# Kernel optimization log

Hardware: AMD Instinct MI355X
Metric: run time of the kernel (lower is better)

## Reference

```python
import jax, jax.numpy as jnp
import numpy as np
import math

B, S, H = 2, 2048, 2048
NH, HD = 32, 64
BASE, SCALE = 10000.0, 2.0
MAX_POS, ORIG_MAX_POS = 8192, 8192
BETA_FAST, BETA_SLOW = 32, 1
EPS = 1e-6


def _yarn_cos_sin():
    # revised_yarn: scale inv_freq by 1/((1-mask)*scale + mask)
    inv_freq = 1.0 / BASE ** (np.arange(0, HD, 2, dtype=np.float64) / HD)
    def corr(nr):
        return HD * math.log(ORIG_MAX_POS / (nr * 2 * math.pi)) / (2 * math.log(BASE))
    low = max(math.floor(corr(BETA_FAST)), 0)
    high = min(math.ceil(corr(BETA_SLOW)), HD - 1)
    hi = high + 0.001 if low == high else high
    ramp = np.clip((np.arange(HD // 2, dtype=np.float64) - low) / (hi - low), 0.0, 1.0)
    mask = 1.0 - ramp  # extrapolation_factor = 1
    inv_freq = inv_freq / ((1.0 - mask) * SCALE + mask)
    mscale = (0.1 * math.log(SCALE) + 1.0) if SCALE > 1 else 1.0
    t = np.arange(MAX_POS, dtype=np.float64)
    freqs = np.outer(t, inv_freq)
    emb = np.concatenate([freqs, freqs], axis=-1)
    return np.cos(emb) * mscale, np.sin(emb) * mscale

_COS_NP, _SIN_NP = _yarn_cos_sin()


def rotate_half(x):
    x1, x2 = jnp.split(x, 2, axis=-1)
    return jnp.concatenate([-x2, x1], axis=-1)


def rms_norm(x, w):
    v = jnp.mean(jnp.square(x.astype(jnp.float32)), axis=-1, keepdims=True)
    return (x.astype(jnp.float32) * jax.lax.rsqrt(v + EPS)).astype(x.dtype) * w


def localized_filtering(x, lf1, lf2, w1, b1, w2, b2, ln_w):
    # x: (B,S,H); torch works in (B,H,S,1) with kernel-(2,1) convs over seq
    residual = x
    xi = jnp.transpose(x, (0, 2, 1))[:, :, :, None]  # (B,H,S,1)
    xi = jnp.concatenate([lf1, xi], axis=2)          # (B,H,S+1,1)
    dn = ('NCHW', 'OIHW', 'NCHW')
    o1 = jax.lax.conv_general_dilated(xi, w1, (1, 1), 'VALID', dimension_numbers=dn)
    o1 = o1 + b1[None, :, None, None]                # (B,H/2,S,1)
    o1c = jnp.concatenate([lf2, o1], axis=2)         # (B,H/2,S+1,1)
    o2 = jax.lax.conv_general_dilated(o1c, w2, (1, 1), 'VALID', dimension_numbers=dn)
    o2 = o2 + b2[None, :, None, None]                # (B,H,S,1)
    o2 = jnp.transpose(o2[:, :, :, 0], (0, 2, 1))    # (B,S,H)
    return rms_norm(o2 + residual, ln_w)


def setup_inputs():
    key = jax.random.key(0)
    ks = jax.random.split(key, 8)
    f = lambda k, shp: jax.random.normal(k, shp, dtype=jnp.float32) * 0.02
    return {
        'hidden_states': jax.random.normal(ks[0], (B, S, H), dtype=jnp.float32),
        'position_ids': jnp.broadcast_to(jnp.arange(S, dtype=jnp.int32)[None, :], (B, S)),
        'lf1_cache': jnp.zeros((B, H, 1, 1), jnp.float32),
        'lf2_cache': jnp.zeros((B, H // 2, 1, 1), jnp.float32),
        'Wqk': f(ks[1], (2 * H, H)),
        'Wv': f(ks[2], (H, H)),
        'Wo': f(ks[3], (H, H)),
        'conv1_w': f(ks[4], (H // 2, H, 2, 1)),
        'conv1_b': jnp.zeros((H // 2,), jnp.float32),
        'conv2_w': f(ks[5], (H, H // 2, 2, 1)),
        'conv2_b': jnp.zeros((H,), jnp.float32),
        'ln_w': jnp.ones((H,), jnp.float32),
    }


def reference(hidden_states, position_ids, lf1_cache, lf2_cache, Wqk, Wv, Wo,
              conv1_w, conv1_b, conv2_w, conv2_b, ln_w):
    cos = jnp.asarray(_COS_NP, jnp.float32)
    sin = jnp.asarray(_SIN_NP, jnp.float32)
    # v from raw hidden states
    v = (hidden_states @ Wv.T).reshape(B, S, NH, HD).transpose(0, 2, 1, 3)  # (B,NH,S,HD)
    # localized filtering gate feeds q/k projection
    lf = localized_filtering(hidden_states, lf1_cache, lf2_cache,
                             conv1_w, conv1_b, conv2_w, conv2_b, ln_w)
    qk = (lf @ Wqk.T).reshape(B, S, NH, 2 * HD)  # per-head [q|k] split
    q = qk[..., :HD].transpose(0, 2, 1, 3)       # (B,NH,S,HD)
    k = qk[..., HD:].transpose(0, 2, 1, 3)
    cos_p = cos[position_ids][:, None, :, :]     # (B,1,S,HD)
    sin_p = sin[position_ids][:, None, :, :]
    q = q * cos_p + rotate_half(q) * sin_p
    k = k * cos_p + rotate_half(k) * sin_p
    scores = jnp.einsum('bhqd,bhkd->bhqk', q, k) / math.sqrt(HD)
    causal = jnp.tril(jnp.ones((S, S), dtype=bool))
    scores = jnp.where(causal[None, None], scores, jnp.finfo(scores.dtype).min)
    attn = jax.nn.softmax(scores, axis=-1)
    ctx = jnp.einsum('bhqk,bhkd->bhqd', attn, v)
    out = ctx.transpose(0, 2, 1, 3).reshape(B, S, H) @ Wo.T
    return out
```

## Files before the change

### kernel.cpp

```cpp
#include <hip/hip_runtime.h>
#include <hip/hip_bf16.h>
#include <math.h>
#include <stdint.h>

typedef __hip_bfloat16 bf16;
using f32x4 = __attribute__((ext_vector_type(4))) float;
using s16x8 = __attribute__((ext_vector_type(8))) short;

constexpr int Bc = 2, Sc = 2048, Hc = 2048, NHc = 32, HDc = 64;
constexpr int Mc = Bc * Sc;
constexpr int MAXPOS = 8192;

constexpr size_t OFF_WV  = 0;
constexpr size_t OFF_WQK = OFF_WV  + (size_t)Hc * Hc * 2;
constexpr size_t OFF_WO  = OFF_WQK + (size_t)2 * Hc * Hc * 2;
constexpr size_t OFF_W1  = OFF_WO  + (size_t)Hc * Hc * 2;
constexpr size_t OFF_W2  = OFF_W1  + (size_t)(Hc/2) * (2*Hc) * 2;
constexpr size_t OFF_HS  = OFF_W2  + (size_t)Hc * Hc * 2;
constexpr size_t OFF_XPR = OFF_HS  + (size_t)Mc * Hc * 2;
constexpr size_t OFF_O1  = OFF_XPR + (size_t)Mc * Hc * 2;
constexpr size_t OFF_O1P = OFF_O1  + (size_t)Mc * (Hc/2) * 2;
constexpr size_t OFF_O2  = OFF_O1P + (size_t)Mc * (Hc/2) * 2;
constexpr size_t OFF_LF  = OFF_O2  + (size_t)Mc * Hc * 4;
constexpr size_t OFF_VT  = OFF_LF  + (size_t)Mc * Hc * 2;
constexpr size_t OFF_COS = OFF_VT  + (size_t)Mc * Hc * 2;
constexpr size_t OFF_SIN = OFF_COS + (size_t)MAXPOS * HDc * 4;
constexpr size_t OFF_Q   = OFF_XPR;
constexpr size_t OFF_K   = OFF_HS;
constexpr size_t OFF_CTX = OFF_O1;

__device__ __forceinline__ f32x4 mfma16(s16x8 a, s16x8 b, f32x4 c) {
  return __builtin_amdgcn_mfma_f32_16x16x32_bf16(a, b, c, 0, 0, 0);
}
__device__ __forceinline__ void gload16(const bf16* g, bf16* l) {
  __builtin_amdgcn_global_load_lds(
      (__attribute__((address_space(1))) void*)g,
      (__attribute__((address_space(3))) void*)l, 16, 0, 0);
}
__device__ __forceinline__ uint16_t bfbits(float x) {
  union { bf16 h; uint16_t u; } v; v.h = __float2bfloat16(x); return v.u;
}
__device__ __forceinline__ uint32_t pkbf(float a, float b) {
  return (uint32_t)bfbits(a) | ((uint32_t)bfbits(b) << 16);
}
__device__ __forceinline__ void block_bar() {
  asm volatile("" ::: "memory");
  __builtin_amdgcn_s_barrier();
  asm volatile("" ::: "memory");
}
template <int N> __device__ __forceinline__ void vm_wait() {
  if constexpr (N == 0)      asm volatile("s_waitcnt vmcnt(0)" ::: "memory");
  else if constexpr (N == 2) asm volatile("s_waitcnt vmcnt(2)" ::: "memory");
  else if constexpr (N == 3) asm volatile("s_waitcnt vmcnt(3)" ::: "memory");
  else if constexpr (N == 4) asm volatile("s_waitcnt vmcnt(4)" ::: "memory");
  else if constexpr (N == 6) asm volatile("s_waitcnt vmcnt(6)" ::: "memory");
  else if constexpr (N == 8) asm volatile("s_waitcnt vmcnt(8)" ::: "memory");
}

__global__ void k_cvt(const float* __restrict__ in, bf16* __restrict__ out, int n) {
  int i = blockIdx.x * 256 + threadIdx.x;
  if (i < n) out[i] = __float2bfloat16(in[i]);
}

__global__ void k_cvt_hs(const float* __restrict__ hs, const float* __restrict__ lf1,
                         bf16* __restrict__ hsb, bf16* __restrict__ xprev) {
  int i = blockIdx.x * 256 + threadIdx.x;
  if (i >= Mc * Hc) return;
  float v = hs[i];
  bf16 b = __float2bfloat16(v);
  hsb[i] = b;
  int row = i >> 11, col = i & (Hc - 1);
  int s = row & (Sc - 1), bb = row >> 11;
  if (s + 1 < Sc) xprev[i + Hc] = b;
  if (s == 0)     xprev[i] = __float2bfloat16(lf1[bb * Hc + col]);
}

__global__ void k_repack1(const float* __restrict__ w, bf16* __restrict__ out) {
  int i = blockIdx.x * 256 + threadIdx.x;
  if (i >= (Hc/2) * 2 * Hc) return;
  int oc = i >> 12, k = i & 4095;
  int ic = k & (Hc - 1), t = k >> 11;
  out[i] = __float2bfloat16(w[((size_t)oc * Hc + ic) * 2 + t]);
}
__global__ void k_repack2(const float* __restrict__ w, bf16* __restrict__ out) {
  int i = blockIdx.x * 256 + threadIdx.x;
  if (i >= Hc * Hc) return;
  int c = i >> 11, k = i & (Hc - 1);
  int oc = k & (Hc/2 - 1), t = k >> 10;
  out[i] = __float2bfloat16(w[((size_t)c * (Hc/2) + oc) * 2 + t]);
}

__global__ void k_prefill_o1p(const float* __restrict__ lf2, bf16* __restrict__ o1p) {
  int i = blockIdx.x * 256 + threadIdx.x;
  if (i >= Bc * (Hc/2)) return;
  int b = i >> 10, n = i & (Hc/2 - 1);
  o1p[(size_t)b * Sc * (Hc/2) + n] = __float2bfloat16(lf2[i]);
}

struct InvF { double v[32]; double mscale; };

__global__ void k_costab(InvF f, float* __restrict__ ct, float* __restrict__ st) {
  int i = blockIdx.x * 256 + threadIdx.x;
  if (i >= MAXPOS * HDc) return;
  int p = i >> 6, d = i & 63;
  double ang = (double)p * f.v[d & 31];
  ct[i] = (float)(cos(ang) * f.mscale);
  st[i] = (float)(sin(ang) * f.mscale);
}

__global__ __launch_bounds__(256) void k_rmsnorm(const float* __restrict__ x,
                                                 const float* __restrict__ w,
                                                 bf16* __restrict__ out) {
  __shared__ float red[4];
  int row = blockIdx.x;
  const float* xr = x + (size_t)row * Hc;
  float ss = 0.f;
  for (int c = threadIdx.x; c < Hc; c += 256) { float v = xr[c]; ss += v * v; }
  for (int off = 32; off; off >>= 1) ss += __shfl_down(ss, off, 64);
  if ((threadIdx.x & 63) == 0) red[threadIdx.x >> 6] = ss;
  __syncthreads();
  float sc = rsqrtf((red[0] + red[1] + red[2] + red[3]) / Hc + 1e-6f);
  for (int c = threadIdx.x; c < Hc; c += 256)
    out[(size_t)row * Hc + c] = __float2bfloat16(xr[c] * sc * w[c]);
}

template <int EPI, int BM, int BN>
__global__ __launch_bounds__(512, 2) void gemm8(
    const bf16* __restrict__ A0, const bf16* __restrict__ A1, int Ksplit,
    const bf16* __restrict__ Bw, int K, int N, void* __restrict__ Cout,
    const float* __restrict__ bias, const float* __restrict__ resid,
    const int* __restrict__ pos, const float* __restrict__ ct,
    const float* __restrict__ st, bf16* __restrict__ out2) {
  constexpr int L = (BM + BN) / 128;
  constexpr int TILE = (BM + BN) * 32;
  constexpr int MF = (BM == 256) ? ((BN == 256) ? 8 : 4) : 4;
  constexpr int NF = (BN == 256) ? 4 : ((BM == 256) ? 4 : 2);
  __shared__ __align__(16) bf16 lds[3][TILE];
  const int tid = threadIdx.x;
  const int w = tid >> 6, l = tid & 63;
  const int lrow = l & 15, lg = l >> 4;
  const int wm = (BM == 256) ? ((BN == 256) ? (w >> 2) * 128 : (w & 3) * 64)
                             : (w >> 2) * 64;
  const int wn = (BM == 256) ? ((BN == 256) ? (w & 3) * 64 : (w >> 2) * 64)
                             : (w & 3) * 32;
  const int gx = gridDim.x;
  const int lin = blockIdx.y * gx + blockIdx.x;
  const int cx = gx >> 2, cy = gridDim.y >> 1;
  const int c = lin & 7, idx = lin >> 3;
  const int bn = (c & 3) * cx + idx % cx;
  const int bm = (c >> 2) * cy + idx / cx;

  auto ld1 = [&](const bf16* srcbase, size_t stride, bf16* ldst, int ci) {
    const int pr = ci >> 3, rem = ci & 7;
    const int r = pr * 2 + (rem >> 2), g = (rem & 3) ^ (pr & 3);
    gload16(srcbase + (size_t)r * stride + g * 8, ldst + ci * 8);
  };
  auto stage = [&](int kt, int slot) {
    const int kcol = kt * 32;
    const bf16* Au; int kc;
    if (kcol < Ksplit) { Au = A0; kc = kcol; } else { Au = A1; kc = kcol - Ksplit; }
    const bf16* As_ = Au + (size_t)bm * BM * Ksplit + kc;
    bf16* ldsA = lds[slot];
    ld1(As_, Ksplit, ldsA, tid);
    if constexpr (BM == 256) ld1(As_, Ksplit, ldsA, tid + 512);
    const bf16* Bs_ = Bw + (size_t)bn * BN * K + kcol;
    bf16* ldsB = lds[slot] + BM * 32;
    ld1(Bs_, K, ldsB, tid);
    if constexpr (BN == 256) ld1(Bs_, K, ldsB, tid + 512);
  };
  auto frag = [&](const bf16* base, int r) -> s16x8 {
    const int s = ((r >> 1) << 3) + ((r & 1) << 2) + (lg ^ ((r >> 1) & 3));
    return *(const s16x8*)(base + s * 8);
  };

  f32x4 acc[MF][NF] = {};
  const int nkt = K / 32;
  stage(0, 0);
  stage(1, 1);
  for (int t = 0; t < nkt; ++t) {
    if (t + 2 < nkt) { stage(t + 2, (t + 2) % 3); vm_wait<2 * L>(); }
    else if (t + 1 < nkt) { vm_wait<L>(); }
    else { vm_wait<0>(); }
    block_bar();
    const bf16* Asl = lds[t % 3];
    const bf16* Bsl = Asl + BM * 32;
    s16x8 af[MF], bfr[NF];
#pragma unroll
    for (int m = 0; m < MF; ++m) af[m] = frag(Asl, wm + m * 16 + lrow);
#pragma unroll
    for (int n = 0; n < NF; ++n) bfr[n] = frag(Bsl, wn + n * 16 + lrow);
    __builtin_amdgcn_s_setprio(1);
#pragma unroll
    for (int m = 0; m < MF; ++m)
#pragma unroll
      for (int n = 0; n < NF; ++n)
        acc[m][n] = mfma16(af[m], bfr[n], acc[m][n]);
    __builtin_amdgcn_s_setprio(0);
    block_bar();
  }
  if constexpr (EPI == 6) {
    const int gcol0 = bn * BN + wn;
    const int h = gcol0 >> 7, half = (gcol0 >> 6) & 1;
    bf16* outp = half ? out2 : (bf16*)Cout;
    const float qsc = half ? 1.0f : 0.125f * 1.44269504088896f;
#pragma unroll
    for (int m = 0; m < MF; ++m)
#pragma unroll
      for (int r = 0; r < 4; ++r) {
        const int grow = bm * BM + wm + m * 16 + lg * 4 + r;
        const int p = pos[grow];
        const int bb = grow >> 11, s = grow & (Sc - 1);
        bf16* rowp = outp + ((size_t)(bb * NHc + h) * Sc + s) * 64;
#pragma unroll
        for (int n = 0; n < 2; ++n) {
          const int dd = n * 16 + lrow;
          const float c0 = ct[p * 64 + dd],      s0 = st[p * 64 + dd];
          const float c1 = ct[p * 64 + 32 + dd], s1 = st[p * 64 + 32 + dd];
          const float v0 = acc[m][n][r], v1 = acc[m][n + 2][r];
          rowp[dd]      = __float2bfloat16((v0 * c0 - v1 * s0) * qsc);
          rowp[dd + 32] = __float2bfloat16((v1 * c1 + v0 * s1) * qsc);
        }
      }
  } else {
#pragma unroll
    for (int m = 0; m < MF; ++m)
#pragma unroll
      for (int n = 0; n < NF; ++n)
#pragma unroll
        for (int r = 0; r < 4; ++r) {
          const int grow = bm * BM + wm + m * 16 + lg * 4 + r;
          const int gcol = bn * BN + wn + n * 16 + lrow;
          float v = acc[m][n][r];
          if constexpr (EPI == 1) {
            v += bias[gcol];
            bf16 bv = __float2bfloat16(v);
            ((bf16*)Cout)[(size_t)grow * N + gcol] = bv;
            if ((grow & (Sc - 1)) != Sc - 1) out2[(size_t)(grow + 1) * N + gcol] = bv;
          } else if constexpr (EPI == 2) {
            v += bias[gcol] + resid[(size_t)grow * N + gcol];
            ((float*)Cout)[(size_t)grow * N + gcol] = v;
          } else if constexpr (EPI == 5) {
            const int b = gcol >> 11, s = gcol & (Sc - 1);
            ((bf16*)Cout)[((size_t)(b * Hc + grow)) * Sc + s] = __float2bfloat16(v);
          } else {
            ((float*)Cout)[(size_t)grow * N + gcol] = v;
          }
        }
  }
}

__global__ __launch_bounds__(256) void k_attn(const bf16* __restrict__ Q,
                                              const bf16* __restrict__ Kg,
                                              const bf16* __restrict__ Vt,
                                              bf16* __restrict__ ctx) {
  __shared__ __align__(16) bf16 Ks[2][64 * 64];
  __shared__ __align__(16) bf16 Vs[2][64 * 64];
  __shared__ __align__(16) uint32_t Pl[4][2][2][16][20];
  const int tid = threadIdx.x;
  const int w = tid >> 6, l = tid & 63;
  const int lrow = l & 15, lg = l >> 4, lk = lg * 8;
  const int bh = blockIdx.x;
  const int tile = blockIdx.y;
  const bf16* Qp = Q  + (size_t)bh * Sc * HDc;
  const bf16* Kp = Kg + (size_t)bh * Sc * HDc;
  const bf16* Vp = Vt + (size_t)bh * HDc * Sc;
  const int b = bh >> 5, h = bh & 31;
  const s16x8 ones8 = {16256, 16256, 16256, 16256, 16256, 16256, 16256, 16256};

  const int srow0 = tid >> 3, schunk = tid & 7;

  for (int pass = 0; pass < 2; ++pass) {
    const int base = (pass == 0) ? tile * 128 : (Sc - 128 - tile * 128);
    const int q0 = base + w * 32;
    const int NT = base / 64 + 2;

    s16x8 qa[2][2];
#pragma unroll
    for (int m = 0; m < 2; ++m)
#pragma unroll
      for (int hf = 0; hf < 2; ++hf)
        qa[m][hf] = *(const s16x8*)&Qp[(size_t)(q0 + m * 16 + lrow) * 64 + hf * 32 + lk];

    f32x4 o[2][4] = {};
    f32x4 lsf[2] = {};
    float mx[2] = {-1e30f, -1e30f};

    {
      gload16(Kp + (size_t)srow0 * 64 + ((schunk ^ (srow0 & 7)) << 3), &Ks[0][tid * 8]);
      gload16(Kp + (size_t)(32 + srow0) * 64 + ((schunk ^ ((32 + srow0) & 7)) << 3),
              &Ks[0][2048 + tid * 8]);
      gload16(Vp + (size_t)srow0 * Sc + ((schunk ^ (srow0 & 7)) << 3), &Vs[0][tid * 8]);
      gload16(Vp + (size_t)(32 + srow0) * Sc + ((schunk ^ ((32 + srow0) & 7)) << 3),
              &Vs[0][2048 + tid * 8]);
    }
    __syncthreads();

    for (int t = 0; t < NT; ++t) {
      const int cur = t & 1;
      const int kv0 = t * 64;
      if (t + 1 < NT) {
        const int nkv = kv0 + 64;
        const int nb = cur ^ 1;
        gload16(Kp + (size_t)(nkv + srow0) * 64 + ((schunk ^ (srow0 & 7)) << 3),
                &Ks[nb][tid * 8]);
        gload16(Kp + (size_t)(nkv + 32 + srow0) * 64 + ((schunk ^ ((32 + srow0) & 7)) << 3),
                &Ks[nb][2048 + tid * 8]);
        gload16(Vp + (size_t)srow0 * Sc + nkv + ((schunk ^ (srow0 & 7)) << 3),
                &Vs[nb][tid * 8]);
        gload16(Vp + (size_t)(32 + srow0) * Sc + nkv + ((schunk ^ ((32 + srow0) & 7)) << 3),
                &Vs[nb][2048 + tid * 8]);
      }
      if (kv0 <= q0) {
        s16x8 kc[8], vc[4][2];
#pragma unroll
        for (int c = 0; c < 4; ++c)
#pragma unroll
          for (int hf = 0; hf < 2; ++hf) {
            const int row = c * 16 + lrow;
            kc[c * 2 + hf] =
                *(const s16x8*)&Ks[cur][row * 64 + (((hf << 2) + lg) ^ (row & 7)) * 8];
          }
#pragma unroll
        for (int db = 0; db < 4; ++db)
#pragma unroll
          for (int kh = 0; kh < 2; ++kh) {
            const int row = db * 16 + lrow;
            vc[db][kh] =
                *(const s16x8*)&Vs[cur][row * 64 + (((kh << 2) + lg) ^ (row & 7)) * 8];
          }
        const bool lastit = (kv0 + 64 > q0);

#pragma unroll
        for (int m = 0; m < 2; ++m) {
          f32x4 s[4];
          __builtin_amdgcn_s_setprio(1);
#pragma unroll
          for (int c = 0; c < 4; ++c) {
            f32x4 z = {};
            z = mfma16(kc[c * 2], qa[m][0], z);
            z = mfma16(kc[c * 2 + 1], qa[m][1], z);
            s[c] = z;
          }
          __builtin_amdgcn_s_setprio(0);

          if (lastit) {
            const int qq = q0 + m * 16 + lrow;
#pragma unroll
            for (int c = 0; c < 4; ++c)
#pragma unroll
              for (int r = 0; r < 4; ++r)
                if (kv0 + c * 16 + lg * 4 + r > qq) s[c][r] = -1e30f;
          }
          float t16 = fmaxf(
              fmaxf(fmaxf(fmaxf(s[0][0], s[0][1]), fmaxf(s[0][2], s[0][3])),
                    fmaxf(fmaxf(s[1][0], s[1][1]), fmaxf(s[1][2], s[1][3]))),
              fmaxf(fmaxf(fmaxf(s[2][0], s[2][1]), fmaxf(s[2][2], s[2][3])),
                    fmaxf(fmaxf(s[3][0], s[3][1]), fmaxf(s[3][2], s[3][3]))));
          if (!__all(t16 <= mx[m] + 8.0f)) {
            t16 = fmaxf(t16, __shfl_xor(t16, 16, 64));
            t16 = fmaxf(t16, __shfl_xor(t16, 32, 64));
            const float mnew = fmaxf(mx[m], t16);
            const float sold = __builtin_amdgcn_exp2f(mx[m] - mnew);
            mx[m] = mnew;
            lsf[m] *= sold;
#pragma unroll
            for (int db = 0; db < 4; ++db) o[m][db] *= sold;
          }
          float p[4][4];
#pragma unroll
          for (int c = 0; c < 4; ++c)
#pragma unroll
            for (int r = 0; r < 4; ++r)
              p[c][r] = __builtin_amdgcn_exp2f(s[c][r] - mx[m]);
#pragma unroll
          for (int kh = 0; kh < 2; ++kh) {
            *(uint64_t*)&Pl[w][m][kh][lrow][lg * 2] =
                (uint64_t)pkbf(p[kh * 2][0], p[kh * 2][1]) |
                ((uint64_t)pkbf(p[kh * 2][2], p[kh * 2][3]) << 32);
            *(uint64_t*)&Pl[w][m][kh][lrow][8 + lg * 2] =
                (uint64_t)pkbf(p[kh * 2 + 1][0], p[kh * 2 + 1][1]) |
                ((uint64_t)pkbf(p[kh * 2 + 1][2], p[kh * 2 + 1][3]) << 32);
          }
          const s16x8 pb0 = *(const s16x8*)&Pl[w][m][0][lrow][lg * 4];
          const s16x8 pb1 = *(const s16x8*)&Pl[w][m][1][lrow][lg * 4];
          __builtin_amdgcn_s_setprio(1);
#pragma unroll
          for (int db = 0; db < 4; ++db) o[m][db] = mfma16(vc[db][0], pb0, o[m][db]);
          lsf[m] = mfma16(ones8, pb0, lsf[m]);
#pragma unroll
          for (int db = 0; db < 4; ++db) o[m][db] = mfma16(vc[db][1], pb1, o[m][db]);
          lsf[m] = mfma16(ones8, pb1, lsf[m]);
          __builtin_amdgcn_s_setprio(0);
        }
      }
      __syncthreads();
    }
#pragma unroll
    for (int m = 0; m < 2; ++m) {
      const float inv = 1.0f / lsf[m][0];
      const int qrow = q0 + m * 16 + lrow;
      const size_t rowoff = ((size_t)(b * Sc + qrow)) * Hc + h * 64;
#pragma unroll
      for (int db = 0; db < 4; ++db) {
        uint64_t pk = (uint64_t)bfbits(o[m][db][0] * inv) |
                      ((uint64_t)bfbits(o[m][db][1] * inv) << 16) |
                      ((uint64_t)bfbits(o[m][db][2] * inv) << 32) |
                      ((uint64_t)bfbits(o[m][db][3] * inv) << 48);
        *(uint64_t*)&ctx[rowoff + db * 16 + lg * 4] = pk;
      }
    }
    __syncthreads();
  }
}

extern "C" void kernel_launch(void* const* d_in, const int* in_sizes, int n_in,
                              void* d_out, int out_size, void* d_ws, size_t ws_size,
                              hipStream_t stream) {
  (void)in_sizes; (void)n_in; (void)out_size; (void)ws_size;
  const float* hs  = (const float*)d_in[0];
  const int*   pos = (const int*)d_in[1];
  const float* lf1 = (const float*)d_in[2];
  const float* lf2 = (const float*)d_in[3];
  const float* Wqk = (const float*)d_in[4];
  const float* Wv  = (const float*)d_in[5];
  const float* Wo  = (const float*)d_in[6];
  const float* c1w = (const float*)d_in[7];
  const float* c1b = (const float*)d_in[8];
  const float* c2w = (const float*)d_in[9];
  const float* c2b = (const float*)d_in[10];
  const float* lnw = (const float*)d_in[11];
  float* out = (float*)d_out;
  char*  ws  = (char*)d_ws;

  bf16* wvB   = (bf16*)(ws + OFF_WV);
  bf16* wqkB  = (bf16*)(ws + OFF_WQK);
  bf16* woB   = (bf16*)(ws + OFF_WO);
  bf16* w1B   = (bf16*)(ws + OFF_W1);
  bf16* w2B   = (bf16*)(ws + OFF_W2);
  bf16* hsB   = (bf16*)(ws + OFF_HS);
  bf16* xprB  = (bf16*)(ws + OFF_XPR);
  bf16* o1B   = (bf16*)(ws + OFF_O1);
  bf16* o1pB  = (bf16*)(ws + OFF_O1P);
  float* o2F  = (float*)(ws + OFF_O2);
  bf16* lfB   = (bf16*)(ws + OFF_LF);
  bf16* vtB   = (bf16*)(ws + OFF_VT);
  float* cosT = (float*)(ws + OFF_COS);
  float* sinT = (float*)(ws + OFF_SIN);
  bf16* qB    = (bf16*)(ws + OFF_Q);
  bf16* kB    = (bf16*)(ws + OFF_K);
  bf16* ctxB  = (bf16*)(ws + OFF_CTX);

  InvF f;
  {
    const double base = 10000.0, scale = 2.0;
    const int hd = HDc;
    auto corr = [&](double nr) {
      return hd * log(8192.0 / (nr * 2.0 * M_PI)) / (2.0 * log(base));
    };
    double low = floor(corr(32.0)); if (low < 0) low = 0;
    double high = ceil(corr(1.0));  if (high > hd - 1) high = hd - 1;
    double hi = (low == high) ? high + 0.001 : high;
    for (int i = 0; i < 32; ++i) {
      double inv = 1.0 / pow(base, (2.0 * i) / hd);
      double ramp = ((double)i - low) / (hi - low);
      ramp = ramp < 0.0 ? 0.0 : (ramp > 1.0 ? 1.0 : ramp);
      double mask = 1.0 - ramp;
      f.v[i] = inv / ((1.0 - mask) * scale + mask);
    }
    f.mscale = 0.1 * log(scale) + 1.0;
  }

  k_cvt<<<(Hc * Hc + 255) / 256, 256, 0, stream>>>(Wv, wvB, Hc * Hc);
  k_cvt<<<(2 * Hc * Hc + 255) / 256, 256, 0, stream>>>(Wqk, wqkB, 2 * Hc * Hc);
  k_cvt<<<(Hc * Hc + 255) / 256, 256, 0, stream>>>(Wo, woB, Hc * Hc);
  k_repack1<<<((Hc / 2) * 2 * Hc + 255) / 256, 256, 0, stream>>>(c1w, w1B);
  k_repack2<<<(Hc * Hc + 255) / 256, 256, 0, stream>>>(c2w, w2B);
  k_cvt_hs<<<(Mc * Hc + 255) / 256, 256, 0, stream>>>(hs, lf1, hsB, xprB);
  k_prefill_o1p<<<(Bc * (Hc / 2) + 255) / 256, 256, 0, stream>>>(lf2, o1pB);
  k_costab<<<(MAXPOS * HDc + 255) / 256, 256, 0, stream>>>(f, cosT, sinT);

  gemm8<1, 128, 128><<<dim3((Hc / 2) / 128, Mc / 128), 512, 0, stream>>>(
      xprB, hsB, Hc, w1B, 2 * Hc, Hc / 2, o1B, c1b, nullptr,
      nullptr, nullptr, nullptr, o1pB);
  gemm8<5, 256, 128><<<dim3(Mc / 128, Hc / 256), 512, 0, stream>>>(
      wvB, wvB, Hc, hsB, Hc, Mc, vtB, nullptr, nullptr, nullptr, nullptr, nullptr, nullptr);
  gemm8<2, 256, 128><<<dim3(Hc / 128, Mc / 256), 512, 0, stream>>>(
      o1pB, o1B, Hc / 2, w2B, Hc, Hc, o2F, c2b, hs, nullptr, nullptr, nullptr, nullptr);
  k_rmsnorm<<<Mc, 256, 0, stream>>>(o2F, lnw, lfB);
  gemm8<6, 256, 256><<<dim3((2 * Hc) / 256, Mc / 256), 512, 0, stream>>>(
      lfB, lfB, Hc, wqkB, Hc, 2 * Hc, qB, nullptr, nullptr, pos, cosT, sinT, kB);
  k_attn<<<dim3(64, 8), 256, 0, stream>>>(qB, kB, vtB, ctxB);
  gemm8<4, 256, 128><<<dim3(Hc / 128, Mc / 256), 512, 0, stream>>>(
      ctxB, ctxB, Hc, woB, Hc, Hc, out, nullptr, nullptr, nullptr, nullptr, nullptr, nullptr);
}
```

Before: 451.7 us.

## Merge prep kernels, vectorize conversions, bf16 residual path, dedicated QK RoPE GEMM

Eight preprocessing launches are merged into one k_prep kernel, and the hidden-state conversion is vectorized to four elements per thread. The conv2 output and its residual now use bf16 instead of fp32, taking the residual from the bf16 copy of hidden_states, and rmsnorm reads that bf16 with vectorized loads and stores. The QK projection with RoPE moves into a dedicated gemm_q8 kernel with 64-wide K steps, double buffering and an 8-slot XOR swizzle. The aim is to cut launch overhead and memory traffic, at the cost of extra rounding in the residual and normalization inputs.

```diff
diff --git a/kernel.cpp b/kernel.cpp
--- a/kernel.cpp
+++ b/kernel.cpp
@@ -40,8 +40,14 @@
 __device__ __forceinline__ uint16_t bfbits(float x) {
   union { bf16 h; uint16_t u; } v; v.h = __float2bfloat16(x); return v.u;
 }
+__device__ __forceinline__ float bff(uint16_t u) {
+  union { bf16 h; uint16_t u; } v; v.u = u; return __bfloat162float(v.h);
+}
 __device__ __forceinline__ uint32_t pkbf(float a, float b) {
   return (uint32_t)bfbits(a) | ((uint32_t)bfbits(b) << 16);
+}
+__device__ __forceinline__ uint64_t pkbf4(float a, float b, float c, float d) {
+  return (uint64_t)pkbf(a, b) | ((uint64_t)pkbf(c, d) << 32);
 }
 __device__ __forceinline__ void block_bar() {
   asm volatile("" ::: "memory");
@@ -57,92 +63,107 @@
   else if constexpr (N == 8) asm volatile("s_waitcnt vmcnt(8)" ::: "memory");
 }
 
-__global__ void k_cvt(const float* __restrict__ in, bf16* __restrict__ out, int n) {
-  int i = blockIdx.x * 256 + threadIdx.x;
-  if (i < n) out[i] = __float2bfloat16(in[i]);
-}
-
-__global__ void k_cvt_hs(const float* __restrict__ hs, const float* __restrict__ lf1,
-                         bf16* __restrict__ hsb, bf16* __restrict__ xprev) {
-  int i = blockIdx.x * 256 + threadIdx.x;
+struct InvF { double v[32]; double mscale; };
+
+__global__ void k_prep(const float* __restrict__ Wv, const float* __restrict__ Wqk,
+                       const float* __restrict__ Wo, const float* __restrict__ c1w,
+                       const float* __restrict__ c2w, const float* __restrict__ lf2,
+                       InvF f, bf16* __restrict__ wv, bf16* __restrict__ wqk,
+                       bf16* __restrict__ wo, bf16* __restrict__ w1,
+                       bf16* __restrict__ w2, bf16* __restrict__ o1p,
+                       float* __restrict__ ct, float* __restrict__ st) {
+  const int blk = blockIdx.x, tid = threadIdx.x;
+  if (blk < 16384) {
+    const int i = blk * 256 + tid;
+    wv[i] = __float2bfloat16(Wv[i]);
+  } else if (blk < 49152) {
+    const int i = (blk - 16384) * 256 + tid;
+    wqk[i] = __float2bfloat16(Wqk[i]);
+  } else if (blk < 65536) {
+    const int i = (blk - 49152) * 256 + tid;
+    wo[i] = __float2bfloat16(Wo[i]);
+  } else if (blk < 81920) {
+    const int i = (blk - 65536) * 256 + tid;
+    const int oc = i >> 12, k = i & 4095;
+    const int ic = k & (Hc - 1), t = k >> 11;
+    w1[i] = __float2bfloat16(c1w[((size_t)oc * Hc + ic) * 2 + t]);
+  } else if (blk < 98304) {
+    const int i = (blk - 81920) * 256 + tid;
+    const int c = i >> 11, k = i & (Hc - 1);
+    const int oc = k & (Hc / 2 - 1), t = k >> 10;
+    w2[i] = __float2bfloat16(c2w[((size_t)c * (Hc / 2) + oc) * 2 + t]);
+  } else if (blk < 100352) {
+    const int i = (blk - 98304) * 256 + tid;
+    const int p = i >> 6, d = i & 63;
+    const double ang = (double)p * f.v[d & 31];
+    ct[i] = (float)(cos(ang) * f.mscale);
+    st[i] = (float)(sin(ang) * f.mscale);
+  } else {
+    const int i = (blk - 100352) * 256 + tid;
+    if (i < Bc * (Hc / 2)) {
+      const int b = i >> 10, n = i & (Hc / 2 - 1);
+      o1p[(size_t)b * Sc * (Hc / 2) + n] = __float2bfloat16(lf2[i]);
+    }
+  }
+}
+
+__global__ void k_cvt_hs4(const float* __restrict__ hs, const float* __restrict__ lf1,
+                          bf16* __restrict__ hsb, bf16* __restrict__ xprev) {
+  const int i = (blockIdx.x * 256 + threadIdx.x) * 4;
   if (i >= Mc * Hc) return;
-  float v = hs[i];
-  bf16 b = __float2bfloat16(v);
-  hsb[i] = b;
-  int row = i >> 11, col = i & (Hc - 1);
-  int s = row & (Sc - 1), bb = row >> 11;
-  if (s + 1 < Sc) xprev[i + Hc] = b;
-  if (s == 0)     xprev[i] = __float2bfloat16(lf1[bb * Hc + col]);
-}
-
-__global__ void k_repack1(const float* __restrict__ w, bf16* __restrict__ out) {
-  int i = blockIdx.x * 256 + threadIdx.x;
-  if (i >= (Hc/2) * 2 * Hc) return;
-  int oc = i >> 12, k = i & 4095;
-  int ic = k & (Hc - 1), t = k >> 11;
-  out[i] = __float2bfloat16(w[((size_t)oc * Hc + ic) * 2 + t]);
-}
-__global__ void k_repack2(const float* __restrict__ w, bf16* __restrict__ out) {
-  int i = blockIdx.x * 256 + threadIdx.x;
-  if (i >= Hc * Hc) return;
-  int c = i >> 11, k = i & (Hc - 1);
-  int oc = k & (Hc/2 - 1), t = k >> 10;
-  out[i] = __float2bfloat16(w[((size_t)c * (Hc/2) + oc) * 2 + t]);
-}
-
-__global__ void k_prefill_o1p(const float* __restrict__ lf2, bf16* __restrict__ o1p) {
-  int i = blockIdx.x * 256 + threadIdx.x;
-  if (i >= Bc * (Hc/2)) return;
-  int b = i >> 10, n = i & (Hc/2 - 1);
-  o1p[(size_t)b * Sc * (Hc/2) + n] = __float2bfloat16(lf2[i]);
-}
-
-struct InvF { double v[32]; double mscale; };
-
-__global__ void k_costab(InvF f, float* __restrict__ ct, float* __restrict__ st) {
-  int i = blockIdx.x * 256 + threadIdx.x;
-  if (i >= MAXPOS * HDc) return;
-  int p = i >> 6, d = i & 63;
-  double ang = (double)p * f.v[d & 31];
-  ct[i] = (float)(cos(ang) * f.mscale);
-  st[i] = (float)(sin(ang) * f.mscale);
-}
-
-__global__ __launch_bounds__(256) void k_rmsnorm(const float* __restrict__ x,
+  const float4 v = *(const float4*)(hs + i);
+  const uint64_t pk = pkbf4(v.x, v.y, v.z, v.w);
+  *(uint64_t*)(hsb + i) = pk;
+  const int row = i >> 11, s = row & (Sc - 1), bb = row >> 11, col = i & (Hc - 1);
+  if (s + 1 < Sc) *(uint64_t*)(xprev + i + Hc) = pk;
+  if (s == 0) {
+    const float4 lv = *(const float4*)(lf1 + bb * Hc + col);
+    *(uint64_t*)(xprev + i) = pkbf4(lv.x, lv.y, lv.z, lv.w);
+  }
+}
+
+__global__ __launch_bounds__(256) void k_rmsnorm(const bf16* __restrict__ x,
                                                  const float* __restrict__ w,
                                                  bf16* __restrict__ out) {
   __shared__ float red[4];
-  int row = blockIdx.x;
-  const float* xr = x + (size_t)row * Hc;
+  const int row = blockIdx.x, tid = threadIdx.x;
+  const s16x8 v = *(const s16x8*)(x + (size_t)row * Hc + tid * 8);
+  float fv[8];
   float ss = 0.f;
-  for (int c = threadIdx.x; c < Hc; c += 256) { float v = xr[c]; ss += v * v; }
+#pragma unroll
+  for (int j = 0; j < 8; ++j) {
+    fv[j] = bff((uint16_t)v[j]);
+    ss += fv[j] * fv[j];
+  }
   for (int off = 32; off; off >>= 1) ss += __shfl_down(ss, off, 64);
-  if ((threadIdx.x & 63) == 0) red[threadIdx.x >> 6] = ss;
+  if ((tid & 63) == 0) red[tid >> 6] = ss;
   __syncthreads();
-  float sc = rsqrtf((red[0] + red[1] + red[2] + red[3]) / Hc + 1e-6f);
-  for (int c = threadIdx.x; c < Hc; c += 256)
-    out[(size_t)row * Hc + c] = __float2bfloat16(xr[c] * sc * w[c]);
+  const float sc = rsqrtf((red[0] + red[1] + red[2] + red[3]) / Hc + 1e-6f);
+  const float4 w0 = *(const float4*)(w + tid * 8);
+  const float4 w1 = *(const float4*)(w + tid * 8 + 4);
+  uint64_t lo = pkbf4(fv[0] * sc * w0.x, fv[1] * sc * w0.y,
+                      fv[2] * sc * w0.z, fv[3] * sc * w0.w);
+  uint64_t hi = pkbf4(fv[4] * sc * w1.x, fv[5] * sc * w1.y,
+                      fv[6] * sc * w1.z, fv[7] * sc * w1.w);
+  uint64_t* op = (uint64_t*)(out + (size_t)row * Hc + tid * 8);
+  op[0] = lo; op[1] = hi;
 }
 
 template <int EPI, int BM, int BN>
 __global__ __launch_bounds__(512, 2) void gemm8(
     const bf16* __restrict__ A0, const bf16* __restrict__ A1, int Ksplit,
     const bf16* __restrict__ Bw, int K, int N, void* __restrict__ Cout,
-    const float* __restrict__ bias, const float* __restrict__ resid,
-    const int* __restrict__ pos, const float* __restrict__ ct,
-    const float* __restrict__ st, bf16* __restrict__ out2) {
+    const float* __restrict__ bias, bf16* __restrict__ out2) {
   constexpr int L = (BM + BN) / 128;
   constexpr int TILE = (BM + BN) * 32;
-  constexpr int MF = (BM == 256) ? ((BN == 256) ? 8 : 4) : 4;
-  constexpr int NF = (BN == 256) ? 4 : ((BM == 256) ? 4 : 2);
+  constexpr int MF = (BM == 256) ? 4 : 4;
+  constexpr int NF = (BM == 256) ? 4 : 2;
   __shared__ __align__(16) bf16 lds[3][TILE];
   const int tid = threadIdx.x;
   const int w = tid >> 6, l = tid & 63;
   const int lrow = l & 15, lg = l >> 4;
-  const int wm = (BM == 256) ? ((BN == 256) ? (w >> 2) * 128 : (w & 3) * 64)
-                             : (w >> 2) * 64;
-  const int wn = (BM == 256) ? ((BN == 256) ? (w & 3) * 64 : (w >> 2) * 64)
-                             : (w & 3) * 32;
+  const int wm = (BM == 256) ? (w & 3) * 64 : (w >> 2) * 64;
+  const int wn = (BM == 256) ? (w >> 2) * 64 : (w & 3) * 32;
   const int gx = gridDim.x;
   const int lin = blockIdx.y * gx + blockIdx.x;
   const int cx = gx >> 2, cy = gridDim.y >> 1;
@@ -198,55 +219,120 @@
     __builtin_amdgcn_s_setprio(0);
     block_bar();
   }
-  if constexpr (EPI == 6) {
-    const int gcol0 = bn * BN + wn;
-    const int h = gcol0 >> 7, half = (gcol0 >> 6) & 1;
-    bf16* outp = half ? out2 : (bf16*)Cout;
-    const float qsc = half ? 1.0f : 0.125f * 1.44269504088896f;
-#pragma unroll
-    for (int m = 0; m < MF; ++m)
+#pragma unroll
+  for (int m = 0; m < MF; ++m)
+#pragma unroll
+    for (int n = 0; n < NF; ++n)
 #pragma unroll
       for (int r = 0; r < 4; ++r) {
         const int grow = bm * BM + wm + m * 16 + lg * 4 + r;
-        const int p = pos[grow];
-        const int bb = grow >> 11, s = grow & (Sc - 1);
-        bf16* rowp = outp + ((size_t)(bb * NHc + h) * Sc + s) * 64;
-#pragma unroll
-        for (int n = 0; n < 2; ++n) {
-          const int dd = n * 16 + lrow;
-          const float c0 = ct[p * 64 + dd],      s0 = st[p * 64 + dd];
-          const float c1 = ct[p * 64 + 32 + dd], s1 = st[p * 64 + 32 + dd];
-          const float v0 = acc[m][n][r], v1 = acc[m][n + 2][r];
-          rowp[dd]      = __float2bfloat16((v0 * c0 - v1 * s0) * qsc);
-          rowp[dd + 32] = __float2bfloat16((v1 * c1 + v0 * s1) * qsc);
+        const int gcol = bn * BN + wn + n * 16 + lrow;
+        float v = acc[m][n][r];
+        if constexpr (EPI == 1) {
+          v += bias[gcol];
+          bf16 bv = __float2bfloat16(v);
+          ((bf16*)Cout)[(size_t)grow * N + gcol] = bv;
+          if ((grow & (Sc - 1)) != Sc - 1) out2[(size_t)(grow + 1) * N + gcol] = bv;
+        } else if constexpr (EPI == 2) {
+          v += bias[gcol] + __bfloat162float(out2[(size_t)grow * N + gcol]);
+          ((bf16*)Cout)[(size_t)grow * N + gcol] = __float2bfloat16(v);
+        } else if constexpr (EPI == 5) {
+          const int b = gcol >> 11, s = gcol & (Sc - 1);
+          ((bf16*)Cout)[((size_t)(b * Hc + grow)) * Sc + s] = __float2bfloat16(v);
+        } else {
+          ((float*)Cout)[(size_t)grow * N + gcol] = v;
         }
       }
-  } else {
-#pragma unroll
-    for (int m = 0; m < MF; ++m)
-#pragma unroll
-      for (int n = 0; n < NF; ++n)
-#pragma unroll
-        for (int r = 0; r < 4; ++r) {
-          const int grow = bm * BM + wm + m * 16 + lg * 4 + r;
-          const int gcol = bn * BN + wn + n * 16 + lrow;
-          float v = acc[m][n][r];
-          if constexpr (EPI == 1) {
-            v += bias[gcol];
-            bf16 bv = __float2bfloat16(v);
-            ((bf16*)Cout)[(size_t)grow * N + gcol] = bv;
-            if ((grow & (Sc - 1)) != Sc - 1) out2[(size_t)(grow + 1) * N + gcol] = bv;
-          } else if constexpr (EPI == 2) {
-            v += bias[gcol] + resid[(size_t)grow * N + gcol];
-            ((float*)Cout)[(size_t)grow * N + gcol] = v;
-          } else if constexpr (EPI == 5) {
-            const int b = gcol >> 11, s = gcol & (Sc - 1);
-            ((bf16*)Cout)[((size_t)(b * Hc + grow)) * Sc + s] = __float2bfloat16(v);
-          } else {
-            ((float*)Cout)[(size_t)grow * N + gcol] = v;
-          }
-        }
-  }
+}
+
+__global__ __launch_bounds__(512, 2) void gemm_q8(
+    const bf16* __restrict__ A, const bf16* __restrict__ Bw,
+    const int* __restrict__ pos, const float* __restrict__ ct,
+    const float* __restrict__ st, bf16* __restrict__ qout,
+    bf16* __restrict__ kout) {
+  constexpr int K = Hc;
+  __shared__ __align__(16) bf16 lds[2][32768];
+  const int tid = threadIdx.x;
+  const int w = tid >> 6, l = tid & 63;
+  const int lrow = l & 15, lg = l >> 4;
+  const int wm = (w >> 2) * 128, wn = (w & 3) * 64;
+  const int gx = gridDim.x;
+  const int lin = blockIdx.y * gx + blockIdx.x;
+  const int cx = gx >> 2, cy = gridDim.y >> 1;
+  const int c = lin & 7, idx = lin >> 3;
+  const int bn = (c & 3) * cx + idx % cx;
+  const int bm = (c >> 2) * cy + idx / cx;
+
+  auto stage = [&](int kt, int slot) {
+    const int kcol = kt * 64;
+    const bf16* Ab = A + (size_t)bm * 256 * K + kcol;
+    const bf16* Bb = Bw + (size_t)bn * 256 * K + kcol;
+    bf16* dA = lds[slot];
+    bf16* dB = lds[slot] + 16384;
+#pragma unroll
+    for (int j = 0; j < 4; ++j) {
+      const int ci = tid + j * 512;
+      const int r = ci >> 3, g = (ci & 7) ^ (r & 7);
+      gload16(Ab + (size_t)r * K + g * 8, dA + ci * 8);
+    }
+#pragma unroll
+    for (int j = 0; j < 4; ++j) {
+      const int ci = tid + j * 512;
+      const int r = ci >> 3, g = (ci & 7) ^ (r & 7);
+      gload16(Bb + (size_t)r * K + g * 8, dB + ci * 8);
+    }
+  };
+  auto frag = [&](const bf16* base, int r, int kb) -> s16x8 {
+    const int cp = (kb << 2) + lg;
+    return *(const s16x8*)(base + (r * 8 + (cp ^ (r & 7))) * 8);
+  };
+
+  f32x4 acc[8][4] = {};
+  stage(0, 0);
+  for (int t = 0; t < K / 64; ++t) {
+    if (t + 1 < K / 64) { stage(t + 1, (t + 1) & 1); vm_wait<8>(); }
+    else { vm_wait<0>(); }
+    block_bar();
+    const bf16* Asl = lds[t & 1];
+    const bf16* Bsl = Asl + 16384;
+#pragma unroll
+    for (int kb = 0; kb < 2; ++kb) {
+      s16x8 bfr[4];
+#pragma unroll
+      for (int n = 0; n < 4; ++n) bfr[n] = frag(Bsl, wn + n * 16 + lrow, kb);
+      __builtin_amdgcn_s_setprio(1);
+#pragma unroll
+      for (int m = 0; m < 8; ++m) {
+        const s16x8 af = frag(Asl, wm + m * 16 + lrow, kb);
+#pragma unroll
+        for (int n = 0; n < 4; ++n) acc[m][n] = mfma16(af, bfr[n], acc[m][n]);
+      }
+      __builtin_amdgcn_s_setprio(0);
+    }
+    block_bar();
+  }
+  const int gcol0 = bn * 256 + wn;
+  const int h = gcol0 >> 7, half = (gcol0 >> 6) & 1;
+  bf16* outp = half ? kout : qout;
+  const float qsc = half ? 1.0f : 0.125f * 1.44269504088896f;
+#pragma unroll
+  for (int m = 0; m < 8; ++m)
+#pragma unroll
+    for (int r = 0; r < 4; ++r) {
+      const int grow = bm * 256 + wm + m * 16 + lg * 4 + r;
+      const int p = pos[grow];
+      const int bb = grow >> 11, s = grow & (Sc - 1);
+      bf16* rowp = outp + ((size_t)(bb * NHc + h) * Sc + s) * 64;
+#pragma unroll
+      for (int n = 0; n < 2; ++n) {
+        const int dd = n * 16 + lrow;
+        const float c0 = ct[p * 64 + dd],      s0 = st[p * 64 + dd];
+        const float c1 = ct[p * 64 + 32 + dd], s1 = st[p * 64 + 32 + dd];
+        const float v0 = acc[m][n][r], v1 = acc[m][n + 2][r];
+        rowp[dd]      = __float2bfloat16((v0 * c0 - v1 * s0) * qsc);
+        rowp[dd + 32] = __float2bfloat16((v1 * c1 + v0 * s1) * qsc);
+      }
+    }
 }
 
 __global__ __launch_bounds__(256) void k_attn(const bf16* __restrict__ Q,
@@ -375,11 +461,10 @@
 #pragma unroll
           for (int kh = 0; kh < 2; ++kh) {
             *(uint64_t*)&Pl[w][m][kh][lrow][lg * 2] =
-                (uint64_t)pkbf(p[kh * 2][0], p[kh * 2][1]) |
-                ((uint64_t)pkbf(p[kh * 2][2], p[kh * 2][3]) << 32);
+                pkbf4(p[kh * 2][0], p[kh * 2][1], p[kh * 2][2], p[kh * 2][3]);
             *(uint64_t*)&Pl[w][m][kh][lrow][8 + lg * 2] =
-                (uint64_t)pkbf(p[kh * 2 + 1][0], p[kh * 2 + 1][1]) |
-                ((uint64_t)pkbf(p[kh * 2 + 1][2], p[kh * 2 + 1][3]) << 32);
+                pkbf4(p[kh * 2 + 1][0], p[kh * 2 + 1][1],
+                      p[kh * 2 + 1][2], p[kh * 2 + 1][3]);
           }
           const s16x8 pb0 = *(const s16x8*)&Pl[w][m][0][lrow][lg * 4];
           const s16x8 pb1 = *(const s16x8*)&Pl[w][m][1][lrow][lg * 4];
@@ -441,7 +526,7 @@
   bf16* xprB  = (bf16*)(ws + OFF_XPR);
   bf16* o1B   = (bf16*)(ws + OFF_O1);
   bf16* o1pB  = (bf16*)(ws + OFF_O1P);
-  float* o2F  = (float*)(ws + OFF_O2);
+  bf16* o2B   = (bf16*)(ws + OFF_O2);
   bf16* lfB   = (bf16*)(ws + OFF_LF);
   bf16* vtB   = (bf16*)(ws + OFF_VT);
   float* cosT = (float*)(ws + OFF_COS);
@@ -470,26 +555,20 @@
     f.mscale = 0.1 * log(scale) + 1.0;
   }
 
-  k_cvt<<<(Hc * Hc + 255) / 256, 256, 0, stream>>>(Wv, wvB, Hc * Hc);
-  k_cvt<<<(2 * Hc * Hc + 255) / 256, 256, 0, stream>>>(Wqk, wqkB, 2 * Hc * Hc);
-  k_cvt<<<(Hc * Hc + 255) / 256, 256, 0, stream>>>(Wo, woB, Hc * Hc);
-  k_repack1<<<((Hc / 2) * 2 * Hc + 255) / 256, 256, 0, stream>>>(c1w, w1B);
-  k_repack2<<<(Hc * Hc + 255) / 256, 256, 0, stream>>>(c2w, w2B);
-  k_cvt_hs<<<(Mc * Hc + 255) / 256, 256, 0, stream>>>(hs, lf1, hsB, xprB);
-  k_prefill_o1p<<<(Bc * (Hc / 2) + 255) / 256, 256, 0, stream>>>(lf2, o1pB);
-  k_costab<<<(MAXPOS * HDc + 255) / 256, 256, 0, stream>>>(f, cosT, sinT);
+  k_prep<<<100360, 256, 0, stream>>>(Wv, Wqk, Wo, c1w, c2w, lf2, f,
+                                     wvB, wqkB, woB, w1B, w2B, o1pB, cosT, sinT);
+  k_cvt_hs4<<<(Mc * Hc / 4 + 255) / 256, 256, 0, stream>>>(hs, lf1, hsB, xprB);
 
   gemm8<1, 128, 128><<<dim3((Hc / 2) / 128, Mc / 128), 512, 0, stream>>>(
-      xprB, hsB, Hc, w1B, 2 * Hc, Hc / 2, o1B, c1b, nullptr,
-      nullptr, nullptr, nullptr, o1pB);
+      xprB, hsB, Hc, w1B, 2 * Hc, Hc / 2, o1B, c1b, o1pB);
   gemm8<5, 256, 128><<<dim3(Mc / 128, Hc / 256), 512, 0, stream>>>(
-      wvB, wvB, Hc, hsB, Hc, Mc, vtB, nullptr, nullptr, nullptr, nullptr, nullptr, nullptr);
+      wvB, wvB, Hc, hsB, Hc, Mc, vtB, nullptr, nullptr);
   gemm8<2, 256, 128><<<dim3(Hc / 128, Mc / 256), 512, 0, stream>>>(
-      o1pB, o1B, Hc / 2, w2B, Hc, Hc, o2F, c2b, hs, nullptr, nullptr, nullptr, nullptr);
-  k_rmsnorm<<<Mc, 256, 0, stream>>>(o2F, lnw, lfB);
-  gemm8<6, 256, 256><<<dim3((2 * Hc) / 256, Mc / 256), 512, 0, stream>>>(
-      lfB, lfB, Hc, wqkB, Hc, 2 * Hc, qB, nullptr, nullptr, pos, cosT, sinT, kB);
+      o1pB, o1B, Hc / 2, w2B, Hc, Hc, o2B, c2b, hsB);
+  k_rmsnorm<<<Mc, 256, 0, stream>>>(o2B, lnw, lfB);
+  gemm_q8<<<dim3((2 * Hc) / 256, Mc / 256), 512, 0, stream>>>(
+      lfB, wqkB, pos, cosT, sinT, qB, kB);
   k_attn<<<dim3(64, 8), 256, 0, stream>>>(qB, kB, vtB, ctxB);
   gemm8<4, 256, 128><<<dim3(Hc / 128, Mc / 256), 512, 0, stream>>>(
-      ctxB, ctxB, Hc, woB, Hc, Hc, out, nullptr, nullptr, nullptr, nullptr, nullptr, nullptr);
-}
+      ctxB, ctxB, Hc, woB, Hc, Hc, out, nullptr, nullptr);
+}
```

Measured after the change: 405.5 us (median of 3 runs). 10.2% less time.
